# Optimization experiments

Measured on AMD Instinct MI355X. Metric: run time of the kernel, lower is better.

## Reference

```python
import jax, jax.numpy as jnp
import numpy as np
import math

D_MODEL = 2048
NUM_HEADS = 16
QUERY_GROUPS = 4
HEAD_DIM = D_MODEL // NUM_HEADS  # 128
B, T = 2, 2048


def setup_inputs() -> dict:
    key = jax.random.key(0)
    ks = jax.random.split(key, 9)
    s = 0.02
    return {
        "x": jax.random.normal(ks[0], (B, T, D_MODEL), dtype=jnp.float32),
        "Wq": jax.random.normal(ks[1], (D_MODEL, NUM_HEADS * HEAD_DIM), dtype=jnp.float32) * s,
        "bq": jnp.zeros((NUM_HEADS * HEAD_DIM,), dtype=jnp.float32),
        "Wk": jax.random.normal(ks[2], (D_MODEL, QUERY_GROUPS * HEAD_DIM), dtype=jnp.float32) * s,
        "bk": jnp.zeros((QUERY_GROUPS * HEAD_DIM,), dtype=jnp.float32),
        "Wv": jax.random.normal(ks[3], (D_MODEL, QUERY_GROUPS * HEAD_DIM), dtype=jnp.float32) * s,
        "bv": jnp.zeros((QUERY_GROUPS * HEAD_DIM,), dtype=jnp.float32),
        "Wo": jax.random.normal(ks[4], (D_MODEL, D_MODEL), dtype=jnp.float32) * s,
        "bo": jnp.zeros((D_MODEL,), dtype=jnp.float32),
    }


def reference(x, Wq, bq, Wk, bk, Wv, bv, Wo, bo):
    Bb, Tt, Dd = x.shape
    G, H, hd = QUERY_GROUPS, NUM_HEADS, HEAD_DIM
    m = H // G  # heads per group
    # projections
    q = (x @ Wq + bq).reshape(Bb, Tt, G, m, hd)   # [B,T,G,m,hd]
    k = (x @ Wk + bk).reshape(Bb, Tt, G, hd)      # [B,T,G,hd]
    v = (x @ Wv + bv).reshape(Bb, Tt, G, hd)
    # scores with native group broadcast (no explicit K/V expansion)
    scores = jnp.einsum('btgmd,bsgd->bgmts', q, k) / math.sqrt(hd)  # [B,G,m,T,T]
    p = jax.nn.softmax(scores, axis=-1)
    out = jnp.einsum('bgmts,bsgd->btgmd', p, v).reshape(Bb, Tt, Dd)
    # output projection (dropout is identity in eval / p=0)
    return out @ Wo + bo
```

## Files before the change

kernel.cpp:

```cpp
#include <hip/hip_runtime.h>

#define D_MODEL 2048
#define T_SEQ   2048
#define NBATCH  2
#define NH      16
#define NG      4
#define HD      128
#define NQKV    3072

typedef short bf16x8 __attribute__((ext_vector_type(8)));
typedef float f32x4  __attribute__((ext_vector_type(4)));
typedef float f32x16 __attribute__((ext_vector_type(16)));
typedef short s16x4  __attribute__((ext_vector_type(4)));
typedef unsigned u32x4 __attribute__((ext_vector_type(4)));

__device__ __forceinline__ short f2bf(float f) {
  union { float f; unsigned u; } v; v.f = f;
  unsigned r = v.u + 0x7fffu + ((v.u >> 16) & 1u);
  return (short)(r >> 16);
}

__device__ __forceinline__ float bf2f(short s) {
  union { unsigned u; float f; } v; v.u = ((unsigned)(unsigned short)s) << 16;
  return v.f;
}

__device__ __forceinline__ float fast_exp2(float x) {
#if __has_builtin(__builtin_amdgcn_exp2f)
  return __builtin_amdgcn_exp2f(x);
#else
  return __expf(x * 0.6931471805599453f);
#endif
}

__device__ __forceinline__ unsigned cvt_pk_bf16(float a, float b) {
  unsigned r;
  asm("v_cvt_pk_bf16_f32 %0, %1, %2" : "=v"(r) : "v"(a), "v"(b));
  return r;
}

__device__ __forceinline__ void permlane32_swap(unsigned &a, unsigned &b) {
  asm("v_permlane32_swap_b32 %0, %1" : "+v"(a), "+v"(b));
}

__device__ __forceinline__ void gload16(const void* g, void* l) {
  __builtin_amdgcn_global_load_lds(
      (const __attribute__((address_space(1))) void*)g,
      (__attribute__((address_space(3))) void*)l, 16, 0, 0);
}

__global__ __launch_bounds__(256) void convert_x_kernel(
    const float* __restrict__ x, short* __restrict__ o, int n) {
  int i = (blockIdx.x * 256 + threadIdx.x) * 4;
  if (i >= n) return;
  float4 v = *(const float4*)(x + i);
  s16x4 s;
  s[0] = f2bf(v.x); s[1] = f2bf(v.y); s[2] = f2bf(v.z); s[3] = f2bf(v.w);
  *(s16x4*)(o + i) = s;
}

__global__ __launch_bounds__(256) void wtrans_kernel(
    const float* __restrict__ W, short* __restrict__ dst,
    int K, int N, int rowOff, int dstStride) {
  __shared__ float t[32][33];
  int tx = threadIdx.x & 31, ty = threadIdx.x >> 5;
  int kb = blockIdx.x * 32, nb = blockIdx.y * 32;
#pragma unroll
  for (int i = 0; i < 4; ++i)
    t[ty + 8*i][tx] = W[(long)(kb + ty + 8*i) * N + nb + tx];
  __syncthreads();
#pragma unroll
  for (int i = 0; i < 4; ++i)
    dst[(long)(rowOff + nb + ty + 8*i) * dstStride + kb + tx] = f2bf(t[tx][ty + 8*i]);
}

__global__ __launch_bounds__(256) void vtrans_kernel(
    const short* __restrict__ qkv, short* __restrict__ vt) {
  __shared__ short t[32][33];
  int bg = blockIdx.z; int b = bg >> 2, g = bg & 3;
  int sb = blockIdx.x * 32, db = blockIdx.y * 32;
  int tx = threadIdx.x & 31, ty = threadIdx.x >> 5;
  const short* src = qkv + (long)(b * T_SEQ) * NQKV + D_MODEL + NG * HD + g * HD;
#pragma unroll
  for (int i = 0; i < 4; ++i)
    t[ty + 8*i][tx] = src[(long)(sb + ty + 8*i) * NQKV + db + tx];
  __syncthreads();
  short* dst = vt + ((long)bg * HD + db) * T_SEQ + sb;
#pragma unroll
  for (int i = 0; i < 4; ++i)
    dst[(long)(ty + 8*i) * T_SEQ + tx] = t[tx][ty + 8*i];
}

template <int BN, int MODE>
__global__ __launch_bounds__(512, 2) void gemm256_kernel(
    const short* __restrict__ A, const short* __restrict__ BT,
    const float* __restrict__ b0, const float* __restrict__ b1, const float* __restrict__ b2,
    void* __restrict__ Cout, int M, int N, int K) {
  constexpr int BM = 256, BK = 64;
  constexpr int NFR = BN / 64;
  constexpr int ASZ = BM * BK;
  constexpr int BSZ = BN * BK;
  constexpr int ACH = (ASZ * 2 / 16) / 512;
  constexpr int BCH = (BSZ * 2 / 16) / 512;
  __shared__ __align__(16) short smem[(ASZ + BSZ) * 2];

  const int tid = threadIdx.x;
  const int w = tid >> 6, lane = tid & 63;
  const int l15 = lane & 15, quad = lane >> 4;
  const int wr = w & 1, wc = w >> 1;
  const int nb = blockIdx.x, mb = blockIdx.y;
  const short* Ab = A + (long)mb * BM * K;
  const short* Bb = BT + (long)nb * BN * K;

  f32x4 acc[8][NFR];
#pragma unroll
  for (int i = 0; i < 8; ++i)
#pragma unroll
    for (int j = 0; j < NFR; ++j) acc[i][j] = 0.0f;

  int aoff[ACH], boff[BCH];
#pragma unroll
  for (int i = 0; i < ACH; ++i) {
    int chunk = i * 512 + tid;
    int r = chunk >> 3, c = chunk & 7, gc = c ^ (r & 7);
    aoff[i] = r * K + gc * 8;
  }
#pragma unroll
  for (int i = 0; i < BCH; ++i) {
    int chunk = i * 512 + tid;
    int r = chunk >> 3, c = chunk & 7, gc = c ^ (r & 7);
    boff[i] = r * K + gc * 8;
  }

#pragma unroll
  for (int i = 0; i < ACH; ++i) gload16(Ab + aoff[i], smem + (i * 512 + tid) * 8);
#pragma unroll
  for (int i = 0; i < BCH; ++i) gload16(Bb + boff[i], smem + ASZ + (i * 512 + tid) * 8);

  const int NT = K / BK;
  int cur = 0;
  for (int t = 0; t < NT; ++t) {
    asm volatile("s_waitcnt vmcnt(0)" ::: "memory");
    __builtin_amdgcn_s_barrier();
    asm volatile("" ::: "memory");
    if (t + 1 < NT) {
      const int k0n = (t + 1) * BK;
      short* An = smem + (cur ^ 1) * (ASZ + BSZ);
      short* Bn = An + ASZ;
#pragma unroll
      for (int i = 0; i < ACH; ++i) gload16(Ab + k0n + aoff[i], An + (i * 512 + tid) * 8);
#pragma unroll
      for (int i = 0; i < BCH; ++i) gload16(Bb + k0n + boff[i], Bn + (i * 512 + tid) * 8);
    }
    __builtin_amdgcn_sched_barrier(0);
    const short* As = smem + cur * (ASZ + BSZ);
    const short* Bs = As + ASZ;
#pragma unroll
    for (int ks = 0; ks < 2; ++ks) {
      bf16x8 af[8], bfr[NFR];
#pragma unroll
      for (int i = 0; i < 8; ++i) {
        int r = wr * 128 + i * 16 + l15;
        af[i] = *(const bf16x8*)(As + r * 64 + (((ks * 4 + quad) ^ (r & 7)) * 8));
      }
#pragma unroll
      for (int j = 0; j < NFR; ++j) {
        int r = wc * (NFR * 16) + j * 16 + l15;
        bfr[j] = *(const bf16x8*)(Bs + r * 64 + (((ks * 4 + quad) ^ (r & 7)) * 8));
      }
      __builtin_amdgcn_s_setprio(1);
#pragma unroll
      for (int i = 0; i < 8; ++i)
#pragma unroll
        for (int j = 0; j < NFR; ++j)
          acc[i][j] = __builtin_amdgcn_mfma_f32_16x16x32_bf16(af[i], bfr[j], acc[i][j], 0, 0, 0);
      __builtin_amdgcn_s_setprio(0);
    }
    cur ^= 1;
  }

  float biasv[NFR];
#pragma unroll
  for (int j = 0; j < NFR; ++j) {
    int col = nb * BN + wc * (NFR * 16) + j * 16 + l15;
    float bv;
    if (MODE == 0) {
      if (col < 2048)      bv = b0[col];
      else if (col < 2560) bv = b1[col - 2048];
      else                 bv = b2[col - 2560];
    } else bv = b0[col];
    biasv[j] = bv;
  }
  if (MODE == 0) {
    short* C = (short*)Cout;
#pragma unroll
    for (int i = 0; i < 8; ++i)
#pragma unroll
      for (int j = 0; j < NFR; ++j)
#pragma unroll
        for (int r = 0; r < 4; ++r) {
          int row = mb * BM + wr * 128 + i * 16 + quad * 4 + r;
          int col = nb * BN + wc * (NFR * 16) + j * 16 + l15;
          C[(long)row * N + col] = f2bf(acc[i][j][r] + biasv[j]);
        }
  } else {
    float* C = (float*)Cout;
#pragma unroll
    for (int i = 0; i < 8; ++i)
#pragma unroll
      for (int j = 0; j < NFR; ++j)
#pragma unroll
        for (int r = 0; r < 4; ++r) {
          int row = mb * BM + wr * 128 + i * 16 + quad * 4 + r;
          int col = nb * BN + wc * (NFR * 16) + j * 16 + l15;
          C[(long)row * N + col] = acc[i][j][r] + biasv[j];
        }
  }
}

__global__ __launch_bounds__(256, 2) void attn_kernel(
    const short* __restrict__ qkv, const short* __restrict__ vt,
    short* __restrict__ aout) {
  __shared__ __align__(16) short smem[16384];
  short* Ks = smem;
  short* Vs = smem + 8192;

  const int tid = threadIdx.x;
  const int w = tid >> 6, lane = tid & 63;
  const int l31 = lane & 31, hi = lane >> 5;
  const int qt = blockIdx.x, h = blockIdx.y, b = blockIdx.z;
  const int g = h >> 2;
  const short* qbase = qkv + (long)(b * T_SEQ + qt * 128) * NQKV + h * HD;
  const short* kbase = qkv + (long)(b * T_SEQ) * NQKV + D_MODEL + g * HD;
  const short* vbase = vt + (long)(b * NG + g) * HD * T_SEQ;
  const float QSCALE = 0.08838834764831845f * 1.4426950408889634f;

  int kroff[4], vroff[4], dst[4];
#pragma unroll
  for (int t = 0; t < 4; ++t) {
    int chunk = w * 256 + t * 64 + lane;
    { int r = chunk >> 4, c = chunk & 15, gc = c ^ (r & 15);
      kroff[t] = r * NQKV + gc * 8; }
    { int r = chunk >> 3, c = chunk & 7, gc = c ^ (r & 7);
      vroff[t] = r * T_SEQ + gc * 8; }
    dst[t] = chunk * 8;
  }

  bf16x8 qfrag[8];
  {
    const short* qrow = qbase + (long)(w * 32 + l31) * NQKV + hi * 8;
#pragma unroll
    for (int ks = 0; ks < 8; ++ks) {
      bf16x8 v = *(const bf16x8*)(qrow + ks * 16);
#pragma unroll
      for (int e = 0; e < 8; ++e) v[e] = f2bf(bf2f(v[e]) * QSCALE);
      qfrag[ks] = v;
    }
  }

#pragma unroll
  for (int t = 0; t < 4; ++t) {
    gload16(kbase + kroff[t], Ks + dst[t]);
    gload16(vbase + vroff[t], Vs + dst[t]);
  }

  f32x16 oaccT[4];
#pragma unroll
  for (int i = 0; i < 4; ++i) oaccT[i] = 0.0f;
  float lpart[4] = {0.f, 0.f, 0.f, 0.f};

  __syncthreads();

  bf16x8 kpre[4], vpre[4];
  for (int st = 0; st < T_SEQ / 64; ++st) {
    const bool pf = (st + 1 < T_SEQ / 64);
    if (pf) {
      const short* kb2 = kbase + (long)(st + 1) * 64 * NQKV;
      const short* vb2 = vbase + (st + 1) * 64;
#pragma unroll
      for (int t = 0; t < 4; ++t) {
        kpre[t] = *(const bf16x8*)(kb2 + kroff[t]);
        vpre[t] = *(const bf16x8*)(vb2 + vroff[t]);
      }
    }

    f32x16 sacc[2][2];
    sacc[0][0] = 0.0f; sacc[0][1] = 0.0f; sacc[1][0] = 0.0f; sacc[1][1] = 0.0f;
    __builtin_amdgcn_s_setprio(1);
#pragma unroll
    for (int ks = 0; ks < 8; ++ks) {
#pragma unroll
      for (int sb = 0; sb < 2; ++sb) {
        int srow = sb * 32 + l31;
        bf16x8 a = *(const bf16x8*)(Ks + srow * 128 + (((ks * 2 + hi) ^ (srow & 15)) * 8));
        sacc[sb][ks & 1] = __builtin_amdgcn_mfma_f32_32x32x16_bf16(a, qfrag[ks], sacc[sb][ks & 1], 0, 0, 0);
      }
    }
    __builtin_amdgcn_s_setprio(0);

    float p0[16], p1[16];
#pragma unroll
    for (int r = 0; r < 16; ++r) p0[r] = fast_exp2(sacc[0][0][r] + sacc[0][1][r]);
#pragma unroll
    for (int r = 0; r < 16; ++r) p1[r] = fast_exp2(sacc[1][0][r] + sacc[1][1][r]);
#pragma unroll
    for (int r = 0; r < 16; ++r) lpart[r & 3] += p0[r] + p1[r];

    __builtin_amdgcn_s_setprio(1);
#pragma unroll
    for (int k2 = 0; k2 < 4; ++k2) {
      const float* pp = (k2 & 2) ? p1 : p0;
      const int bo = (k2 & 1) * 8;
      unsigned Pa = cvt_pk_bf16(pp[bo + 0], pp[bo + 1]);
      unsigned Pb = cvt_pk_bf16(pp[bo + 2], pp[bo + 3]);
      unsigned Pc = cvt_pk_bf16(pp[bo + 4], pp[bo + 5]);
      unsigned Pd = cvt_pk_bf16(pp[bo + 6], pp[bo + 7]);
      permlane32_swap(Pa, Pc);
      permlane32_swap(Pb, Pd);
      u32x4 pu; pu[0] = Pa; pu[1] = Pb; pu[2] = Pc; pu[3] = Pd;
      bf16x8 pfr = __builtin_bit_cast(bf16x8, pu);
#pragma unroll
      for (int db = 0; db < 4; ++db) {
        int drow = db * 32 + l31;
        bf16x8 a = *(const bf16x8*)(Vs + drow * 64 + (((k2 * 2 + hi) ^ (drow & 7)) * 8));
        oaccT[db] = __builtin_amdgcn_mfma_f32_32x32x16_bf16(a, pfr, oaccT[db], 0, 0, 0);
      }
    }
    __builtin_amdgcn_s_setprio(0);

    __syncthreads();
    if (pf) {
#pragma unroll
      for (int t = 0; t < 4; ++t) {
        *(bf16x8*)(Ks + dst[t]) = kpre[t];
        *(bf16x8*)(Vs + dst[t]) = vpre[t];
      }
    }
    __syncthreads();
  }

  float lsum = (lpart[0] + lpart[1]) + (lpart[2] + lpart[3]);
  float lfull = lsum + __shfl_xor(lsum, 32);
  float inv = 1.0f / lfull;

  short* Osm = smem;
  const int qrl = w * 32 + l31;
#pragma unroll
  for (int db = 0; db < 4; ++db)
#pragma unroll
    for (int r = 0; r < 16; ++r) {
      int dloc = (r & 3) + 8 * (r >> 2) + 4 * hi;
      int d = db * 32 + dloc;
      int c = d >> 3;
      Osm[qrl * 128 + ((c ^ (qrl & 15)) * 8) + (d & 7)] = f2bf(oaccT[db][r] * inv);
    }
  __syncthreads();

  short* obase = aout + (long)(b * T_SEQ + qt * 128) * D_MODEL + h * HD;
  const int row = tid >> 1, ch = tid & 1;
#pragma unroll
  for (int j = 0; j < 8; ++j) {
    int c2 = ch * 8 + j;
    bf16x8 v = *(const bf16x8*)(Osm + row * 128 + ((c2 ^ (row & 15)) * 8));
    *(bf16x8*)(obase + (long)row * D_MODEL + c2 * 8) = v;
  }
}

extern "C" void kernel_launch(void* const* d_in, const int* in_sizes, int n_in,
                              void* d_out, int out_size, void* d_ws, size_t ws_size,
                              hipStream_t stream) {
  const float* x  = (const float*)d_in[0];
  const float* Wq = (const float*)d_in[1];
  const float* bq = (const float*)d_in[2];
  const float* Wk = (const float*)d_in[3];
  const float* bk = (const float*)d_in[4];
  const float* Wv = (const float*)d_in[5];
  const float* bv = (const float*)d_in[6];
  const float* Wo = (const float*)d_in[7];
  const float* bo = (const float*)d_in[8];

  const long NTOK = (long)NBATCH * T_SEQ;
  short* xb    = (short*)d_ws;
  short* wqkvT = xb + NTOK * D_MODEL;
  short* woT   = wqkvT + (long)NQKV * D_MODEL;
  short* qkvb  = woT + (long)D_MODEL * D_MODEL;
  short* vtb   = qkvb + NTOK * NQKV;
  short* attnb = vtb + (long)NBATCH * NG * HD * T_SEQ;

  int nX = (int)(NTOK * D_MODEL);
  convert_x_kernel<<<nX / (256 * 4), 256, 0, stream>>>(x, xb, nX);
  wtrans_kernel<<<dim3(D_MODEL / 32, D_MODEL / 32), 256, 0, stream>>>(Wq, wqkvT, D_MODEL, D_MODEL, 0, D_MODEL);
  wtrans_kernel<<<dim3(D_MODEL / 32, 512 / 32), 256, 0, stream>>>(Wk, wqkvT, D_MODEL, 512, 2048, D_MODEL);
  wtrans_kernel<<<dim3(D_MODEL / 32, 512 / 32), 256, 0, stream>>>(Wv, wqkvT, D_MODEL, 512, 2560, D_MODEL);
  wtrans_kernel<<<dim3(D_MODEL / 32, D_MODEL / 32), 256, 0, stream>>>(Wo, woT, D_MODEL, D_MODEL, 0, D_MODEL);

  gemm256_kernel<256, 0><<<dim3(NQKV / 256, NTOK / 256), 512, 0, stream>>>(
      xb, wqkvT, bq, bk, bv, (void*)qkvb, (int)NTOK, NQKV, D_MODEL);

  vtrans_kernel<<<dim3(T_SEQ / 32, HD / 32, NBATCH * NG), 256, 0, stream>>>(qkvb, vtb);

  attn_kernel<<<dim3(T_SEQ / 128, NH, NBATCH), 256, 0, stream>>>(qkvb, vtb, attnb);

  gemm256_kernel<128, 1><<<dim3(D_MODEL / 128, NTOK / 256), 512, 0, stream>>>(
      attnb, woT, bo, bo, bo, (void*)d_out, (int)NTOK, D_MODEL, D_MODEL);
}
```

Before: 302.3 us.

## Double-buffer K/V tiles with async LDS loads and software-pipeline QK with PV

Replaces the register-staged single-buffer K/V prefetch with double-buffered LDS tiles filled by direct global-to-LDS loads. The loop is software-pipelined so the QK^T scores for tile t+1 are computed while the softmax and PV for tile t run. This is meant to hide load latency and remove one barrier per iteration. LDS per block doubles to 64KB, which may limit occupancy at 2 blocks/CU, and the extra score accumulators raise register pressure. The s_setprio hints are dropped.

```diff
diff --git a/kernel.cpp b/kernel.cpp
--- a/kernel.cpp
+++ b/kernel.cpp
@@ -221,9 +221,7 @@
 __global__ __launch_bounds__(256, 2) void attn_kernel(
     const short* __restrict__ qkv, const short* __restrict__ vt,
     short* __restrict__ aout) {
-  __shared__ __align__(16) short smem[16384];
-  short* Ks = smem;
-  short* Vs = smem + 8192;
+  __shared__ __align__(16) short smem[32768];
 
   const int tid = threadIdx.x;
   const int w = tid >> 6, lane = tid & 63;
@@ -234,6 +232,7 @@
   const short* kbase = qkv + (long)(b * T_SEQ) * NQKV + D_MODEL + g * HD;
   const short* vbase = vt + (long)(b * NG + g) * HD * T_SEQ;
   const float QSCALE = 0.08838834764831845f * 1.4426950408889634f;
+  const int NT = T_SEQ / 64;
 
   int kroff[4], vroff[4], dst[4];
 #pragma unroll
@@ -258,55 +257,45 @@
     }
   }
 
-#pragma unroll
-  for (int t = 0; t < 4; ++t) {
-    gload16(kbase + kroff[t], Ks + dst[t]);
-    gload16(vbase + vroff[t], Vs + dst[t]);
-  }
-
   f32x16 oaccT[4];
 #pragma unroll
   for (int i = 0; i < 4; ++i) oaccT[i] = 0.0f;
   float lpart[4] = {0.f, 0.f, 0.f, 0.f};
-
-  __syncthreads();
-
-  bf16x8 kpre[4], vpre[4];
-  for (int st = 0; st < T_SEQ / 64; ++st) {
-    const bool pf = (st + 1 < T_SEQ / 64);
-    if (pf) {
-      const short* kb2 = kbase + (long)(st + 1) * 64 * NQKV;
-      const short* vb2 = vbase + (st + 1) * 64;
-#pragma unroll
-      for (int t = 0; t < 4; ++t) {
-        kpre[t] = *(const bf16x8*)(kb2 + kroff[t]);
-        vpre[t] = *(const bf16x8*)(vb2 + vroff[t]);
-      }
-    }
-
-    f32x16 sacc[2][2];
-    sacc[0][0] = 0.0f; sacc[0][1] = 0.0f; sacc[1][0] = 0.0f; sacc[1][1] = 0.0f;
-    __builtin_amdgcn_s_setprio(1);
-#pragma unroll
-    for (int ks = 0; ks < 8; ++ks) {
+  f32x16 sA[2][2], sB[2][2];
+
+  auto issueK = [&](int t) {
+    const short* kb2 = kbase + (long)t * 64 * NQKV;
+    short* Kd = smem + (t & 1) * 8192;
+#pragma unroll
+    for (int tt = 0; tt < 4; ++tt) gload16(kb2 + kroff[tt], Kd + dst[tt]);
+  };
+  auto issueV = [&](int t) {
+    const short* vb2 = vbase + t * 64;
+    short* Vd = smem + 16384 + (t & 1) * 8192;
+#pragma unroll
+    for (int tt = 0; tt < 4; ++tt) gload16(vb2 + vroff[tt], Vd + dst[tt]);
+  };
+  auto qk = [&](int t, f32x16 (&S)[2][2]) {
+    const short* KS = smem + (t & 1) * 8192;
+    S[0][0] = 0.0f; S[0][1] = 0.0f; S[1][0] = 0.0f; S[1][1] = 0.0f;
+#pragma unroll
+    for (int ks = 0; ks < 8; ++ks)
 #pragma unroll
       for (int sb = 0; sb < 2; ++sb) {
         int srow = sb * 32 + l31;
-        bf16x8 a = *(const bf16x8*)(Ks + srow * 128 + (((ks * 2 + hi) ^ (srow & 15)) * 8));
-        sacc[sb][ks & 1] = __builtin_amdgcn_mfma_f32_32x32x16_bf16(a, qfrag[ks], sacc[sb][ks & 1], 0, 0, 0);
+        bf16x8 a = *(const bf16x8*)(KS + srow * 128 + (((ks * 2 + hi) ^ (srow & 15)) * 8));
+        S[sb][ks & 1] = __builtin_amdgcn_mfma_f32_32x32x16_bf16(a, qfrag[ks], S[sb][ks & 1], 0, 0, 0);
       }
-    }
-    __builtin_amdgcn_s_setprio(0);
-
+  };
+  auto fin = [&](int tv, f32x16 (&S)[2][2]) {
+    const short* VS = smem + 16384 + (tv & 1) * 8192;
     float p0[16], p1[16];
 #pragma unroll
-    for (int r = 0; r < 16; ++r) p0[r] = fast_exp2(sacc[0][0][r] + sacc[0][1][r]);
-#pragma unroll
-    for (int r = 0; r < 16; ++r) p1[r] = fast_exp2(sacc[1][0][r] + sacc[1][1][r]);
+    for (int r = 0; r < 16; ++r) p0[r] = fast_exp2(S[0][0][r] + S[0][1][r]);
+#pragma unroll
+    for (int r = 0; r < 16; ++r) p1[r] = fast_exp2(S[1][0][r] + S[1][1][r]);
 #pragma unroll
     for (int r = 0; r < 16; ++r) lpart[r & 3] += p0[r] + p1[r];
-
-    __builtin_amdgcn_s_setprio(1);
 #pragma unroll
     for (int k2 = 0; k2 < 4; ++k2) {
       const float* pp = (k2 & 2) ? p1 : p0;
@@ -322,27 +311,46 @@
 #pragma unroll
       for (int db = 0; db < 4; ++db) {
         int drow = db * 32 + l31;
-        bf16x8 a = *(const bf16x8*)(Vs + drow * 64 + (((k2 * 2 + hi) ^ (drow & 7)) * 8));
+        bf16x8 a = *(const bf16x8*)(VS + drow * 64 + (((k2 * 2 + hi) ^ (drow & 7)) * 8));
         oaccT[db] = __builtin_amdgcn_mfma_f32_32x32x16_bf16(a, pfr, oaccT[db], 0, 0, 0);
       }
     }
-    __builtin_amdgcn_s_setprio(0);
-
-    __syncthreads();
-    if (pf) {
-#pragma unroll
-      for (int t = 0; t < 4; ++t) {
-        *(bf16x8*)(Ks + dst[t]) = kpre[t];
-        *(bf16x8*)(Vs + dst[t]) = vpre[t];
-      }
-    }
-    __syncthreads();
-  }
+  };
+
+  issueK(0);
+  asm volatile("s_waitcnt vmcnt(0)" ::: "memory");
+  __builtin_amdgcn_s_barrier();
+  issueK(1); issueV(0);
+  qk(0, sA);
+  asm volatile("s_waitcnt vmcnt(0)" ::: "memory");
+  __builtin_amdgcn_s_barrier();
+
+  for (int t = 1; t < NT - 1; t += 2) {
+    issueK(t + 1); issueV(t);
+    qk(t, sB);
+    fin(t - 1, sA);
+    asm volatile("s_waitcnt vmcnt(0)" ::: "memory");
+    __builtin_amdgcn_s_barrier();
+
+    issueK(t + 2); issueV(t + 1);
+    qk(t + 1, sA);
+    fin(t, sB);
+    asm volatile("s_waitcnt vmcnt(0)" ::: "memory");
+    __builtin_amdgcn_s_barrier();
+  }
+
+  issueV(NT - 1);
+  qk(NT - 1, sB);
+  fin(NT - 2, sA);
+  asm volatile("s_waitcnt vmcnt(0)" ::: "memory");
+  __builtin_amdgcn_s_barrier();
+  fin(NT - 1, sB);
 
   float lsum = (lpart[0] + lpart[1]) + (lpart[2] + lpart[3]);
   float lfull = lsum + __shfl_xor(lsum, 32);
   float inv = 1.0f / lfull;
 
+  __syncthreads();
   short* Osm = smem;
   const int qrl = w * 32 + l31;
 #pragma unroll
```

After: 347.9 us. 15.1% more time.
